# Kernel tuning notes

Measured on AMD Instinct MI355X. Metric: run time of the kernel, lower is better.

The kernel has to match this reference:

```python
import jax, jax.numpy as jnp
import numpy as np

B, S, HID = 2, 2048, 3072
NH, NKV, HD = 16, 8, 256
N_REP = NH // NKV
BITS, BLK = 4, 128
THETA = 10000.0
NEG = -1e9


def quantize_bfp(x, bits=BITS, block_size=BLK):
    """Block-floating-point quantization: blocks of `block_size` along the last
    (head_dim) axis share one power-of-two exponent; mantissas get `bits` levels
    (sign + bits-1), round-to-nearest."""
    shape = x.shape
    xb = x.reshape(-1, block_size)
    maxabs = jnp.max(jnp.abs(xb), axis=-1, keepdims=True)
    e = jnp.floor(jnp.log2(jnp.maximum(maxabs, 1e-30)))
    scale = jnp.exp2(e - (bits - 2))  # largest mantissa ~ 2^(bits-1)-1 covers maxabs
    qmax = 2.0 ** (bits - 1) - 1.0
    q = jnp.clip(jnp.round(xb / scale), -qmax, qmax) * scale
    q = jnp.where(maxabs > 0, q, 0.0)
    return q.reshape(shape)


def rotate_half(x):
    x1, x2 = jnp.split(x, 2, axis=-1)
    return jnp.concatenate((-x2, x1), axis=-1)


def setup_inputs() -> dict:
    key = jax.random.key(0)
    ks = jax.random.split(key, 5)
    hidden_states = jax.random.normal(ks[0], (B, S, HID), dtype=jnp.float32)
    sd = 0.02
    Wq = jax.random.normal(ks[1], (NH * HD, HID), dtype=jnp.float32) * sd
    Wk = jax.random.normal(ks[2], (NKV * HD, HID), dtype=jnp.float32) * sd
    Wv = jax.random.normal(ks[3], (NKV * HD, HID), dtype=jnp.float32) * sd
    Wo = jax.random.normal(ks[4], (HID, NH * HD), dtype=jnp.float32) * sd
    # rotary tables (HF convention: concat(freqs, freqs))
    pos = jnp.arange(S, dtype=jnp.float32)
    inv_freq = 1.0 / (THETA ** (jnp.arange(0, HD, 2, dtype=jnp.float32) / HD))
    freqs = jnp.einsum('s,d->sd', pos, inv_freq)
    emb = jnp.concatenate((freqs, freqs), axis=-1)  # (S, HD)
    cos = jnp.cos(emb)[None]  # (1, S, HD)
    sin = jnp.sin(emb)[None]
    # additive causal mask (B, 1, S, S)
    causal = jnp.where(jnp.tril(jnp.ones((S, S), dtype=bool)), 0.0, NEG).astype(jnp.float32)
    attention_mask = jnp.broadcast_to(causal[None, None], (B, 1, S, S))
    return {"hidden_states": hidden_states, "Wq": Wq, "Wk": Wk, "Wv": Wv,
            "Wo": Wo, "cos": cos, "sin": sin, "attention_mask": attention_mask}


def reference(hidden_states, Wq, Wk, Wv, Wo, cos, sin, attention_mask):
    b, s, _ = hidden_states.shape
    q = jnp.einsum('bsh,dh->bsd', hidden_states, Wq).reshape(b, s, NH, HD).transpose(0, 2, 1, 3)
    k = jnp.einsum('bsh,dh->bsd', hidden_states, Wk).reshape(b, s, NKV, HD).transpose(0, 2, 1, 3)
    v = jnp.einsum('bsh,dh->bsd', hidden_states, Wv).reshape(b, s, NKV, HD).transpose(0, 2, 1, 3)
    # RoPE (cos/sin unsqueezed at dim 1 -> (1,1,S,HD))
    c, sn = cos[:, None], sin[:, None]
    q = q * c + rotate_half(q) * sn
    k = k * c + rotate_half(k) * sn
    # int4 BFP quantization of keys (along rows of head_dim)
    k = quantize_bfp(k)
    # GQA: repeat kv heads
    k = jnp.repeat(k, N_REP, axis=1)
    v = jnp.repeat(v, N_REP, axis=1)
    scores = jnp.einsum('bhqd,bhkd->bhqk', q, k) / jnp.sqrt(jnp.float32(HD))
    scores = scores + attention_mask
    attn = jax.nn.softmax(scores.astype(jnp.float32), axis=-1).astype(q.dtype)
    out = jnp.einsum('bhqk,bhkd->bhqd', attn, v)
    out = out.transpose(0, 2, 1, 3).reshape(b, s, NH * HD)
    return jnp.einsum('bsd,hd->bsh', out, Wo)
```

## Files before the change

### kernel.cpp

```cpp
#include <hip/hip_runtime.h>
#include <math.h>

#define Bsz 2
#define Ssz 2048
#define HIDs 3072
#define NHs 16
#define NKVs 8
#define HDs 256

typedef _Float16 f16;
typedef _Float16 f16x8 __attribute__((ext_vector_type(8)));
typedef _Float16 f16x4 __attribute__((ext_vector_type(4)));
typedef float f32x4 __attribute__((ext_vector_type(4)));

__device__ __forceinline__ void async16(const f16* g, f16* l) {
    __builtin_amdgcn_global_load_lds(
        (const __attribute__((address_space(1))) void*)g,
        (__attribute__((address_space(3))) void*)l, 16, 0, 0);
}

__device__ __forceinline__ float row_max16(float v) {
    int t;
    t = __builtin_amdgcn_mov_dpp(__float_as_int(v), 0x121, 0xf, 0xf, false);
    v = fmaxf(v, __int_as_float(t));
    t = __builtin_amdgcn_mov_dpp(__float_as_int(v), 0x122, 0xf, 0xf, false);
    v = fmaxf(v, __int_as_float(t));
    t = __builtin_amdgcn_mov_dpp(__float_as_int(v), 0x124, 0xf, 0xf, false);
    v = fmaxf(v, __int_as_float(t));
    t = __builtin_amdgcn_mov_dpp(__float_as_int(v), 0x128, 0xf, 0xf, false);
    v = fmaxf(v, __int_as_float(t));
    return v;
}
__device__ __forceinline__ float row_sum16(float v) {
    int t;
    t = __builtin_amdgcn_mov_dpp(__float_as_int(v), 0x121, 0xf, 0xf, false);
    v = v + __int_as_float(t);
    t = __builtin_amdgcn_mov_dpp(__float_as_int(v), 0x122, 0xf, 0xf, false);
    v = v + __int_as_float(t);
    t = __builtin_amdgcn_mov_dpp(__float_as_int(v), 0x124, 0xf, 0xf, false);
    v = v + __int_as_float(t);
    t = __builtin_amdgcn_mov_dpp(__float_as_int(v), 0x128, 0xf, 0xf, false);
    v = v + __int_as_float(t);
    return v;
}

#define N4_HS  3145728
#define N4_WQ  3145728
#define N4_WK  1572864
#define N4_WV  1572864
#define N4_WO  3145728
#define N4_TOT (N4_HS + N4_WQ + N4_WK + N4_WV + N4_WO)

__global__ void cast_all_kernel(const float4* __restrict__ hs, const float4* __restrict__ wq,
                                const float4* __restrict__ wk, const float4* __restrict__ wv,
                                const float4* __restrict__ wo,
                                f16x4* __restrict__ hs_h, f16x4* __restrict__ wq_h,
                                f16x4* __restrict__ wk_h, f16x4* __restrict__ wv_h,
                                f16x4* __restrict__ wo_h) {
    int i = blockIdx.x * blockDim.x + threadIdx.x;
    const float4* src; f16x4* dst; int off;
    if (i < N4_HS)                       { src = hs; dst = hs_h; off = i; }
    else if (i < N4_HS + N4_WQ)          { src = wq; dst = wq_h; off = i - N4_HS; }
    else if (i < N4_HS + N4_WQ + N4_WK)  { src = wk; dst = wk_h; off = i - (N4_HS + N4_WQ); }
    else if (i < N4_TOT - N4_WO)         { src = wv; dst = wv_h; off = i - (N4_HS + N4_WQ + N4_WK); }
    else                                 { src = wo; dst = wo_h; off = i - (N4_TOT - N4_WO); }
    float4 v = src[off];
    f16x4 r;
    r[0] = (f16)v.x; r[1] = (f16)v.y; r[2] = (f16)v.z; r[3] = (f16)v.w;
    dst[off] = r;
}

__global__ __launch_bounds__(256) void gemm_nt_f16(
    const f16* __restrict__ A, const f16* __restrict__ Bm, float* __restrict__ C,
    int M, int N, int K)
{
    __shared__ __align__(16) f16 As[128 * 32];
    __shared__ __align__(16) f16 Bs[128 * 32];
    const int tid  = threadIdx.x;
    const int wave = tid >> 6, lane = tid & 63;
    const int l15  = lane & 15, quad = lane >> 4;
    const int m0 = blockIdx.y * 128, n0 = blockIdx.x * 128;
    const int wm = (wave >> 1) * 64, wn = (wave & 1) * 64;
    const int srow = wave * 32 + (lane >> 2);
    const int scol = (lane & 3) * 8;

    f32x4 acc[4][4];
    const f32x4 fz = {0.f, 0.f, 0.f, 0.f};
#pragma unroll
    for (int i = 0; i < 4; i++)
#pragma unroll
        for (int j = 0; j < 4; j++) acc[i][j] = fz;

    const f16* Ag0 = A  + (size_t)(m0 + srow) * K + scol;
    const f16* Ag1 = A  + (size_t)(m0 + srow + 16) * K + scol;
    const f16* Bg0 = Bm + (size_t)(n0 + srow) * K + scol;
    const f16* Bg1 = Bm + (size_t)(n0 + srow + 16) * K + scol;
    f16* Al0 = As + (wave * 32) * 32;
    f16* Al1 = As + (wave * 32 + 16) * 32;
    f16* Bl0 = Bs + (wave * 32) * 32;
    f16* Bl1 = Bs + (wave * 32 + 16) * 32;

    for (int k0 = 0; k0 < K; k0 += 32) {
        __syncthreads();
        async16(Ag0 + k0, Al0);
        async16(Ag1 + k0, Al1);
        async16(Bg0 + k0, Bl0);
        async16(Bg1 + k0, Bl1);
        __syncthreads();
        f16x8 af[4], bfr[4];
#pragma unroll
        for (int i = 0; i < 4; i++)
            af[i] = *(const f16x8*)(As + (wm + i * 16 + l15) * 32 + quad * 8);
#pragma unroll
        for (int j = 0; j < 4; j++)
            bfr[j] = *(const f16x8*)(Bs + (wn + j * 16 + l15) * 32 + quad * 8);
#pragma unroll
        for (int i = 0; i < 4; i++)
#pragma unroll
            for (int j = 0; j < 4; j++)
                acc[i][j] = __builtin_amdgcn_mfma_f32_16x16x32_f16(af[i], bfr[j], acc[i][j], 0, 0, 0);
    }
#pragma unroll
    for (int i = 0; i < 4; i++) {
        const int r = m0 + wm + i * 16 + quad * 4;
#pragma unroll
        for (int j = 0; j < 4; j++) {
            const int c = n0 + wn + j * 16 + l15;
#pragma unroll
            for (int rr = 0; rr < 4; rr++)
                C[(size_t)(r + rr) * N + c] = acc[i][j][rr];
        }
    }
}

__global__ void rope_q_kernel(const float* __restrict__ qp, const float* __restrict__ cosb,
                              const float* __restrict__ sinb, f16* __restrict__ qo) {
    const int s = blockIdx.x, h = blockIdx.y, b = blockIdx.z;
    const int d = threadIdx.x;
    const float* row = qp + (size_t)(b * Ssz + s) * (NHs * HDs) + h * HDs;
    float x = row[d];
    float other = (d < 128) ? -row[d + 128] : row[d - 128];
    float val = (x * cosb[s * HDs + d] + other * sinb[s * HDs + d]) * 0.0625f;
    qo[((size_t)(b * NHs + h) * Ssz + s) * HDs + d] = (f16)val;
}

__global__ void rope_quant_k_kernel(const float* __restrict__ kp, const float* __restrict__ cosb,
                                    const float* __restrict__ sinb, f16* __restrict__ ko) {
    const int s = blockIdx.x, h = blockIdx.y, b = blockIdx.z;
    const int d = threadIdx.x;
    const float* row = kp + (size_t)(b * Ssz + s) * (NKVs * HDs) + h * HDs;
    float x = row[d];
    float other = (d < 128) ? -row[d + 128] : row[d - 128];
    float val = x * cosb[s * HDs + d] + other * sinb[s * HDs + d];
    __shared__ float red[256];
    red[d] = fabsf(val);
    __syncthreads();
    for (int off = 64; off >= 1; off >>= 1) {
        if ((d & 127) < off) red[d] = fmaxf(red[d], red[d + off]);
        __syncthreads();
    }
    float maxabs = red[d & 128];
    float out;
    if (maxabs > 0.f) {
        int ex;
        frexpf(maxabs, &ex);
        float scale = ldexpf(1.0f, ex - 3);
        float q = rintf(val / scale);
        q = fminf(7.f, fmaxf(-7.f, q));
        out = q * scale;
    } else out = 0.f;
    ko[((size_t)(b * NKVs + h) * Ssz + s) * HDs + d] = (f16)out;
}

__global__ __launch_bounds__(256) void transpose_v_kernel(
    const float* __restrict__ proj, f16* __restrict__ vt)
{
    const int s0 = blockIdx.x * 64, c0 = blockIdx.y * 64, b = blockIdx.z;
    const int tid = threadIdx.x;
    __shared__ f16 T[64 * 72];
    {
        const int r = tid >> 2, cc = (tid & 3) * 16;
        const float* src = proj + (size_t)(b * Ssz + s0 + r) * (NKVs * HDs) + c0 + cc;
        f16 tmp[16];
#pragma unroll
        for (int q4 = 0; q4 < 4; q4++) {
            float4 v = *(const float4*)(src + q4 * 4);
            tmp[q4 * 4 + 0] = (f16)v.x; tmp[q4 * 4 + 1] = (f16)v.y;
            tmp[q4 * 4 + 2] = (f16)v.z; tmp[q4 * 4 + 3] = (f16)v.w;
        }
        *(f16x8*)(T + r * 72 + cc)     = *(f16x8*)(tmp);
        *(f16x8*)(T + r * 72 + cc + 8) = *(f16x8*)(tmp + 8);
    }
    __syncthreads();
    {
        const int d = tid >> 2, sc = (tid & 3) * 16;
        f16 tmp[16];
#pragma unroll
        for (int j = 0; j < 16; j++) tmp[j] = T[(sc + j) * 72 + d];
        const int col = c0 + d;
        const int kh = col >> 8, dd = col & 255;
        f16* dst = vt + ((size_t)(b * NKVs + kh) * HDs + dd) * Ssz + s0 + sc;
        *(f16x8*)(dst)     = *(f16x8*)(tmp);
        *(f16x8*)(dst + 8) = *(f16x8*)(tmp + 8);
    }
}

__global__ __launch_bounds__(512, 1) void attn_kernel(
    const f16* __restrict__ Q,
    const f16* __restrict__ Kq,
    const f16* __restrict__ Vt,
    f16* __restrict__ O)
{
    const int flat = blockIdx.x;
    const int xcd  = flat & 7;
    const int slot = flat >> 3;
    const int psel = slot >> 4;
    const int pair = (xcd << 1) | psel;
    const int b    = pair >> 3;
    const int kh   = pair & 7;
    const int sub  = slot & 15;
    const int h    = (kh << 1) | (sub >> 3);
    const int qtp  = sub & 7;
    const int c_short = qtp;
    const int c_long  = 15 - qtp;

    const int tid = threadIdx.x;
    const int wave = tid >> 6, lane = tid & 63;
    const int l15 = lane & 15, quad = lane >> 4;
    const int wrow = (wave < 4) ? (c_short * 128 + wave * 32)
                                : (c_long * 128 + (wave - 4) * 32);

    const f16* Qb  = Q  + ((size_t)(b * NHs  + h)  * Ssz) * HDs;
    const f16* Kg  = Kq + ((size_t)(b * NKVs + kh) * Ssz) * HDs;
    const f16* Vtg = Vt + ((size_t)(b * NKVs + kh) * HDs) * Ssz;

    __shared__ __align__(16) f16 Ks[32 * 256];
    __shared__ __align__(16) f16 Vs[256 * 32];
    __shared__ __align__(16) f16 Pl[8 * 32 * 40];
    f16* Pw = Pl + wave * 32 * 40;

    const int k_r  = lane >> 5;
    const int k_c  = lane & 31;
    const int v_r  = lane >> 2;
    const int v_gc = (lane & 3) ^ ((v_r >> 1) & 3);

    f16x8 qf0[8], qf1[8];
    {
        const f16* qrow0 = Qb + (size_t)(wrow + l15) * HDs + quad * 8;
        const f16* qrow1 = qrow0 + (size_t)16 * HDs;
#pragma unroll
        for (int ks = 0; ks < 8; ks++) {
            qf0[ks] = *(const f16x8*)(qrow0 + ks * 32);
            qf1[ks] = *(const f16x8*)(qrow1 + ks * 32);
        }
    }

    const f32x4 fz = {0.f, 0.f, 0.f, 0.f};
    f32x4 accO0[16], accO1[16];
#pragma unroll
    for (int jn = 0; jn < 16; jn++) { accO0[jn] = fz; accO1[jn] = fz; }
    float mrow0[4], mrow1[4], lp0[4], lp1[4];
#pragma unroll
    for (int r = 0; r < 4; r++) { mrow0[r] = -1e30f; mrow1[r] = -1e30f; lp0[r] = 0.f; lp1[r] = 0.f; }

    const int nk = 4 * c_long + 4;
    const int wave_max_row = wrow + 31;
    const int kswz = l15 & 7;
    const int vswz = (l15 >> 1) & 3;

    for (int kt = 0; kt < nk; kt++) {
        const int kvb = kt * 32;
        __syncthreads();
#pragma unroll
        for (int t = 0; t < 2; t++) {
            const int r2 = wave * 4 + t * 2;
            const int gc = k_c ^ ((r2 + k_r) & 7);
            async16(Kg + (size_t)(kvb + r2 + k_r) * 256 + gc * 8, Ks + r2 * 256);
        }
#pragma unroll
        for (int t = 0; t < 2; t++) {
            const int d0 = wave * 32 + t * 16;
            async16(Vtg + (size_t)(d0 + v_r) * Ssz + kvb + v_gc * 8, Vs + d0 * 32);
        }
        __syncthreads();

        if (kvb <= wave_max_row) {
            f32x4 s00 = fz, s01 = fz, s10 = fz, s11 = fz;
#pragma unroll
            for (int ks = 0; ks < 8; ks++) {
                const int cpos = ((ks * 4 + quad) ^ kswz) * 8;
                f16x8 kf0 = *(const f16x8*)(Ks + l15 * 256 + cpos);
                f16x8 kf1 = *(const f16x8*)(Ks + (16 + l15) * 256 + cpos);
                s00 = __builtin_amdgcn_mfma_f32_16x16x32_f16(qf0[ks], kf0, s00, 0, 0, 0);
                s01 = __builtin_amdgcn_mfma_f32_16x16x32_f16(qf0[ks], kf1, s01, 0, 0, 0);
                s10 = __builtin_amdgcn_mfma_f32_16x16x32_f16(qf1[ks], kf0, s10, 0, 0, 0);
                s11 = __builtin_amdgcn_mfma_f32_16x16x32_f16(qf1[ks], kf1, s11, 0, 0, 0);
            }
            float a0[4], a1[4];
            bool need = false;
            const bool diag = (kvb + 31 > wrow);
#pragma unroll
            for (int r = 0; r < 4; r++) {
                float x0 = s00[r], x1 = s01[r];
                const int row0 = wrow + quad * 4 + r;
                if (diag) {
                    if (kvb + l15 > row0)      x0 = -1e30f;
                    if (kvb + 16 + l15 > row0) x1 = -1e30f;
                }
                float rmax = row_max16(fmaxf(x0, x1));
                float mold = mrow0[r];
                bool upd = rmax > mold + 8.f;
                float mnew = upd ? rmax : mold;
                a0[r] = upd ? __expf(mold - rmax) : 1.0f;
                need = need || upd;
                float p0 = __expf(x0 - mnew);
                float p1 = __expf(x1 - mnew);
                lp0[r] = lp0[r] * a0[r] + (p0 + p1);
                mrow0[r] = mnew;
                Pw[(quad * 4 + r) * 40 + l15]      = (f16)p0;
                Pw[(quad * 4 + r) * 40 + 16 + l15] = (f16)p1;
                float y0 = s10[r], y1 = s11[r];
                const int row1 = row0 + 16;
                if (diag) {
                    if (kvb + l15 > row1)      y0 = -1e30f;
                    if (kvb + 16 + l15 > row1) y1 = -1e30f;
                }
                float rmax1 = row_max16(fmaxf(y0, y1));
                float mold1 = mrow1[r];
                bool upd1 = rmax1 > mold1 + 8.f;
                float mnew1 = upd1 ? rmax1 : mold1;
                a1[r] = upd1 ? __expf(mold1 - rmax1) : 1.0f;
                need = need || upd1;
                float q0 = __expf(y0 - mnew1);
                float q1 = __expf(y1 - mnew1);
                lp1[r] = lp1[r] * a1[r] + (q0 + q1);
                mrow1[r] = mnew1;
                Pw[(16 + quad * 4 + r) * 40 + l15]      = (f16)q0;
                Pw[(16 + quad * 4 + r) * 40 + 16 + l15] = (f16)q1;
            }
            if (__any(need)) {
#pragma unroll
                for (int jn = 0; jn < 16; jn++) {
                    f32x4 t0 = accO0[jn], t1 = accO1[jn];
                    t0[0] *= a0[0]; t0[1] *= a0[1]; t0[2] *= a0[2]; t0[3] *= a0[3];
                    t1[0] *= a1[0]; t1[1] *= a1[1]; t1[2] *= a1[2]; t1[3] *= a1[3];
                    accO0[jn] = t0; accO1[jn] = t1;
                }
            }
            f16x8 pf0 = *(const f16x8*)(Pw + l15 * 40 + quad * 8);
            f16x8 pf1 = *(const f16x8*)(Pw + (16 + l15) * 40 + quad * 8);
#pragma unroll
            for (int jn = 0; jn < 16; jn++) {
                f16x8 vf = *(const f16x8*)(Vs + (jn * 16 + l15) * 32 + (quad ^ vswz) * 8);
                accO0[jn] = __builtin_amdgcn_mfma_f32_16x16x32_f16(pf0, vf, accO0[jn], 0, 0, 0);
                accO1[jn] = __builtin_amdgcn_mfma_f32_16x16x32_f16(pf1, vf, accO1[jn], 0, 0, 0);
            }
        }
    }
#pragma unroll
    for (int r = 0; r < 4; r++) {
        const int row0 = wrow + quad * 4 + r;
        const float inv0 = 1.0f / row_sum16(lp0[r]);
        f16* orow0 = O + ((size_t)(b * Ssz) + row0) * (NHs * HDs) + h * HDs;
#pragma unroll
        for (int jn = 0; jn < 16; jn++)
            orow0[jn * 16 + l15] = (f16)(accO0[jn][r] * inv0);
        const int row1 = row0 + 16;
        const float inv1 = 1.0f / row_sum16(lp1[r]);
        f16* orow1 = O + ((size_t)(b * Ssz) + row1) * (NHs * HDs) + h * HDs;
#pragma unroll
        for (int jn = 0; jn < 16; jn++)
            orow1[jn * 16 + l15] = (f16)(accO1[jn][r] * inv1);
    }
}

extern "C" void kernel_launch(void* const* d_in, const int* in_sizes, int n_in,
                              void* d_out, int out_size, void* d_ws, size_t ws_size,
                              hipStream_t stream) {
    const float* hs   = (const float*)d_in[0];
    const float* Wq   = (const float*)d_in[1];
    const float* Wk   = (const float*)d_in[2];
    const float* Wv   = (const float*)d_in[3];
    const float* Wo   = (const float*)d_in[4];
    const float* cosb = (const float*)d_in[5];
    const float* sinb = (const float*)d_in[6];
    float* out = (float*)d_out;

    char* ws = (char*)d_ws;
    f16*   hs_h = (f16*)(ws);
    f16*   wo_h = (f16*)(ws + 25165824);
    float* proj = (float*)(ws + 50331648);
    f16*   q_h  = (f16*)(ws + 117440512);
    f16*   k_h  = (f16*)(ws + 150994944);
    f16*   vt_h = (f16*)(ws + 167772160);
    f16*   ao_h = (f16*)proj;

    cast_all_kernel<<<N4_TOT / 256, 256, 0, stream>>>(
        (const float4*)hs, (const float4*)Wq, (const float4*)Wk,
        (const float4*)Wv, (const float4*)Wo,
        (f16x4*)hs_h, (f16x4*)q_h, (f16x4*)k_h, (f16x4*)vt_h, (f16x4*)wo_h);

    gemm_nt_f16<<<dim3(4096 / 128, 4096 / 128), 256, 0, stream>>>(hs_h, q_h, proj, 4096, 4096, 3072);
    rope_q_kernel<<<dim3(Ssz, NHs, Bsz), 256, 0, stream>>>(proj, cosb, sinb, q_h);
    gemm_nt_f16<<<dim3(2048 / 128, 4096 / 128), 256, 0, stream>>>(hs_h, k_h, proj, 4096, 2048, 3072);
    rope_quant_k_kernel<<<dim3(Ssz, NKVs, Bsz), 256, 0, stream>>>(proj, cosb, sinb, k_h);
    gemm_nt_f16<<<dim3(2048 / 128, 4096 / 128), 256, 0, stream>>>(hs_h, vt_h, proj, 4096, 2048, 3072);
    transpose_v_kernel<<<dim3(Ssz / 64, (NKVs * HDs) / 64, Bsz), 256, 0, stream>>>(proj, vt_h);
    attn_kernel<<<dim3(256, 1, 1), 512, 0, stream>>>(q_h, k_h, vt_h, ao_h);
    gemm_nt_f16<<<dim3(3072 / 128, 4096 / 128), 256, 0, stream>>>(ao_h, wo_h, out, 4096, 3072, 4096);
}
```

Measured before the change: 934.3 us.

## Double-buffer K/V tiles in LDS to overlap async loads with compute

Splits the K and V shared-memory tiles into two buffers and prefetches the next 32-key tile with async global-to-LDS loads while the current tile is processed. This halves the barriers per tile and aims to hide global load latency behind the MFMA and softmax work. LDS use grows by 32 KB per block, which may lower occupancy. nk is always even (4*c_long+4), so the unrolled-by-two loop covers every tile.

```diff
diff --git a/kernel.cpp b/kernel.cpp
--- a/kernel.cpp
+++ b/kernel.cpp
@@ -234,8 +234,10 @@
     const f16* Kg  = Kq + ((size_t)(b * NKVs + kh) * Ssz) * HDs;
     const f16* Vtg = Vt + ((size_t)(b * NKVs + kh) * HDs) * Ssz;
 
-    __shared__ __align__(16) f16 Ks[32 * 256];
-    __shared__ __align__(16) f16 Vs[256 * 32];
+    __shared__ __align__(16) f16 Ks0[32 * 256];
+    __shared__ __align__(16) f16 Ks1[32 * 256];
+    __shared__ __align__(16) f16 Vs0[256 * 32];
+    __shared__ __align__(16) f16 Vs1[256 * 32];
     __shared__ __align__(16) f16 Pl[8 * 32 * 40];
     f16* Pw = Pl + wave * 32 * 40;
 
@@ -244,6 +246,21 @@
     const int v_r  = lane >> 2;
     const int v_gc = (lane & 3) ^ ((v_r >> 1) & 3);
 
+    auto stage = [&](int kt2, f16* Ksd, f16* Vsd) {
+        const int kvb_ = kt2 * 32;
+#pragma unroll
+        for (int t = 0; t < 2; t++) {
+            const int r2 = wave * 4 + t * 2;
+            const int gc = k_c ^ ((r2 + k_r) & 7);
+            async16(Kg + (size_t)(kvb_ + r2 + k_r) * 256 + gc * 8, Ksd + r2 * 256);
+        }
+#pragma unroll
+        for (int t = 0; t < 2; t++) {
+            const int d0 = wave * 32 + t * 16;
+            async16(Vtg + (size_t)(d0 + v_r) * Ssz + kvb_ + v_gc * 8, Vsd + d0 * 32);
+        }
+    };
+
     f16x8 qf0[8], qf1[8];
     {
         const f16* qrow0 = Qb + (size_t)(wrow + l15) * HDs + quad * 8;
@@ -268,95 +285,93 @@
     const int kswz = l15 & 7;
     const int vswz = (l15 >> 1) & 3;
 
-    for (int kt = 0; kt < nk; kt++) {
-        const int kvb = kt * 32;
+    auto compute = [&](int kvb, const f16* Ksc, const f16* Vsc) {
+        f32x4 s00 = fz, s01 = fz, s10 = fz, s11 = fz;
+#pragma unroll
+        for (int ks = 0; ks < 8; ks++) {
+            const int cpos = ((ks * 4 + quad) ^ kswz) * 8;
+            f16x8 kf0 = *(const f16x8*)(Ksc + l15 * 256 + cpos);
+            f16x8 kf1 = *(const f16x8*)(Ksc + (16 + l15) * 256 + cpos);
+            s00 = __builtin_amdgcn_mfma_f32_16x16x32_f16(qf0[ks], kf0, s00, 0, 0, 0);
+            s01 = __builtin_amdgcn_mfma_f32_16x16x32_f16(qf0[ks], kf1, s01, 0, 0, 0);
+            s10 = __builtin_amdgcn_mfma_f32_16x16x32_f16(qf1[ks], kf0, s10, 0, 0, 0);
+            s11 = __builtin_amdgcn_mfma_f32_16x16x32_f16(qf1[ks], kf1, s11, 0, 0, 0);
+        }
+        float a0[4], a1[4];
+        bool need = false;
+        const bool diag = (kvb + 31 > wrow);
+#pragma unroll
+        for (int r = 0; r < 4; r++) {
+            float x0 = s00[r], x1 = s01[r];
+            const int row0 = wrow + quad * 4 + r;
+            if (diag) {
+                if (kvb + l15 > row0)      x0 = -1e30f;
+                if (kvb + 16 + l15 > row0) x1 = -1e30f;
+            }
+            float rmax = row_max16(fmaxf(x0, x1));
+            float mold = mrow0[r];
+            bool upd = rmax > mold + 8.f;
+            float mnew = upd ? rmax : mold;
+            a0[r] = upd ? __expf(mold - rmax) : 1.0f;
+            need = need || upd;
+            float p0 = __expf(x0 - mnew);
+            float p1 = __expf(x1 - mnew);
+            lp0[r] = lp0[r] * a0[r] + (p0 + p1);
+            mrow0[r] = mnew;
+            Pw[(quad * 4 + r) * 40 + l15]      = (f16)p0;
+            Pw[(quad * 4 + r) * 40 + 16 + l15] = (f16)p1;
+            float y0 = s10[r], y1 = s11[r];
+            const int row1 = row0 + 16;
+            if (diag) {
+                if (kvb + l15 > row1)      y0 = -1e30f;
+                if (kvb + 16 + l15 > row1) y1 = -1e30f;
+            }
+            float rmax1 = row_max16(fmaxf(y0, y1));
+            float mold1 = mrow1[r];
+            bool upd1 = rmax1 > mold1 + 8.f;
+            float mnew1 = upd1 ? rmax1 : mold1;
+            a1[r] = upd1 ? __expf(mold1 - rmax1) : 1.0f;
+            need = need || upd1;
+            float q0 = __expf(y0 - mnew1);
+            float q1 = __expf(y1 - mnew1);
+            lp1[r] = lp1[r] * a1[r] + (q0 + q1);
+            mrow1[r] = mnew1;
+            Pw[(16 + quad * 4 + r) * 40 + l15]      = (f16)q0;
+            Pw[(16 + quad * 4 + r) * 40 + 16 + l15] = (f16)q1;
+        }
+        if (__any(need)) {
+#pragma unroll
+            for (int jn = 0; jn < 16; jn++) {
+                f32x4 t0 = accO0[jn], t1 = accO1[jn];
+                t0[0] *= a0[0]; t0[1] *= a0[1]; t0[2] *= a0[2]; t0[3] *= a0[3];
+                t1[0] *= a1[0]; t1[1] *= a1[1]; t1[2] *= a1[2]; t1[3] *= a1[3];
+                accO0[jn] = t0; accO1[jn] = t1;
+            }
+        }
+        f16x8 pf0 = *(const f16x8*)(Pw + l15 * 40 + quad * 8);
+        f16x8 pf1 = *(const f16x8*)(Pw + (16 + l15) * 40 + quad * 8);
+#pragma unroll
+        for (int jn = 0; jn < 16; jn++) {
+            f16x8 vf = *(const f16x8*)(Vsc + (jn * 16 + l15) * 32 + (quad ^ vswz) * 8);
+            accO0[jn] = __builtin_amdgcn_mfma_f32_16x16x32_f16(pf0, vf, accO0[jn], 0, 0, 0);
+            accO1[jn] = __builtin_amdgcn_mfma_f32_16x16x32_f16(pf1, vf, accO1[jn], 0, 0, 0);
+        }
+    };
+
+    stage(0, Ks0, Vs0);
+    __syncthreads();
+
+    for (int kt = 0; kt < nk; kt += 2) {
+        stage(kt + 1, Ks1, Vs1);
+        const int kvb0 = kt * 32;
+        if (kvb0 <= wave_max_row) compute(kvb0, Ks0, Vs0);
         __syncthreads();
-#pragma unroll
-        for (int t = 0; t < 2; t++) {
-            const int r2 = wave * 4 + t * 2;
-            const int gc = k_c ^ ((r2 + k_r) & 7);
-            async16(Kg + (size_t)(kvb + r2 + k_r) * 256 + gc * 8, Ks + r2 * 256);
-        }
-#pragma unroll
-        for (int t = 0; t < 2; t++) {
-            const int d0 = wave * 32 + t * 16;
-            async16(Vtg + (size_t)(d0 + v_r) * Ssz + kvb + v_gc * 8, Vs + d0 * 32);
-        }
+        if (kt + 2 < nk) stage(kt + 2, Ks0, Vs0);
+        const int kvb1 = kvb0 + 32;
+        if (kvb1 <= wave_max_row) compute(kvb1, Ks1, Vs1);
         __syncthreads();
-
-        if (kvb <= wave_max_row) {
-            f32x4 s00 = fz, s01 = fz, s10 = fz, s11 = fz;
-#pragma unroll
-            for (int ks = 0; ks < 8; ks++) {
-                const int cpos = ((ks * 4 + quad) ^ kswz) * 8;
-                f16x8 kf0 = *(const f16x8*)(Ks + l15 * 256 + cpos);
-                f16x8 kf1 = *(const f16x8*)(Ks + (16 + l15) * 256 + cpos);
-                s00 = __builtin_amdgcn_mfma_f32_16x16x32_f16(qf0[ks], kf0, s00, 0, 0, 0);
-                s01 = __builtin_amdgcn_mfma_f32_16x16x32_f16(qf0[ks], kf1, s01, 0, 0, 0);
-                s10 = __builtin_amdgcn_mfma_f32_16x16x32_f16(qf1[ks], kf0, s10, 0, 0, 0);
-                s11 = __builtin_amdgcn_mfma_f32_16x16x32_f16(qf1[ks], kf1, s11, 0, 0, 0);
-            }
-            float a0[4], a1[4];
-            bool need = false;
-            const bool diag = (kvb + 31 > wrow);
-#pragma unroll
-            for (int r = 0; r < 4; r++) {
-                float x0 = s00[r], x1 = s01[r];
-                const int row0 = wrow + quad * 4 + r;
-                if (diag) {
-                    if (kvb + l15 > row0)      x0 = -1e30f;
-                    if (kvb + 16 + l15 > row0) x1 = -1e30f;
-                }
-                float rmax = row_max16(fmaxf(x0, x1));
-                float mold = mrow0[r];
-                bool upd = rmax > mold + 8.f;
-                float mnew = upd ? rmax : mold;
-                a0[r] = upd ? __expf(mold - rmax) : 1.0f;
-                need = need || upd;
-                float p0 = __expf(x0 - mnew);
-                float p1 = __expf(x1 - mnew);
-                lp0[r] = lp0[r] * a0[r] + (p0 + p1);
-                mrow0[r] = mnew;
-                Pw[(quad * 4 + r) * 40 + l15]      = (f16)p0;
-                Pw[(quad * 4 + r) * 40 + 16 + l15] = (f16)p1;
-                float y0 = s10[r], y1 = s11[r];
-                const int row1 = row0 + 16;
-                if (diag) {
-                    if (kvb + l15 > row1)      y0 = -1e30f;
-                    if (kvb + 16 + l15 > row1) y1 = -1e30f;
-                }
-                float rmax1 = row_max16(fmaxf(y0, y1));
-                float mold1 = mrow1[r];
-                bool upd1 = rmax1 > mold1 + 8.f;
-                float mnew1 = upd1 ? rmax1 : mold1;
-                a1[r] = upd1 ? __expf(mold1 - rmax1) : 1.0f;
-                need = need || upd1;
-                float q0 = __expf(y0 - mnew1);
-                float q1 = __expf(y1 - mnew1);
-                lp1[r] = lp1[r] * a1[r] + (q0 + q1);
-                mrow1[r] = mnew1;
-                Pw[(16 + quad * 4 + r) * 40 + l15]      = (f16)q0;
-                Pw[(16 + quad * 4 + r) * 40 + 16 + l15] = (f16)q1;
-            }
-            if (__any(need)) {
-#pragma unroll
-                for (int jn = 0; jn < 16; jn++) {
-                    f32x4 t0 = accO0[jn], t1 = accO1[jn];
-                    t0[0] *= a0[0]; t0[1] *= a0[1]; t0[2] *= a0[2]; t0[3] *= a0[3];
-                    t1[0] *= a1[0]; t1[1] *= a1[1]; t1[2] *= a1[2]; t1[3] *= a1[3];
-                    accO0[jn] = t0; accO1[jn] = t1;
-                }
-            }
-            f16x8 pf0 = *(const f16x8*)(Pw + l15 * 40 + quad * 8);
-            f16x8 pf1 = *(const f16x8*)(Pw + (16 + l15) * 40 + quad * 8);
-#pragma unroll
-            for (int jn = 0; jn < 16; jn++) {
-                f16x8 vf = *(const f16x8*)(Vs + (jn * 16 + l15) * 32 + (quad ^ vswz) * 8);
-                accO0[jn] = __builtin_amdgcn_mfma_f32_16x16x32_f16(pf0, vf, accO0[jn], 0, 0, 0);
-                accO1[jn] = __builtin_amdgcn_mfma_f32_16x16x32_f16(pf1, vf, accO1[jn], 0, 0, 0);
-            }
-        }
-    }
+    }
+
 #pragma unroll
     for (int r = 0; r < 4; r++) {
         const int row0 = wrow + quad * 4 + r;
```

After: 966.6 us. 1.03x slower.

## Prefetch next K/V tile into registers during attention compute

Applied to the files above, without the earlier changes.

Replaces the direct global-to-LDS async loads of each K/V tile with a register-staged software pipeline. The next tile is loaded into registers while the current tile is computed, then written to LDS after the barrier. The aim is to hide global memory latency behind the MFMA work instead of stalling at the barrier each iteration. The cost is extra VGPRs, which may lower occupancy, plus explicit LDS store instructions.

```diff
diff --git a/kernel.cpp b/kernel.cpp
--- a/kernel.cpp
+++ b/kernel.cpp
@@ -244,6 +244,35 @@
     const int v_r  = lane >> 2;
     const int v_gc = (lane & 3) ^ ((v_r >> 1) & 3);
 
+    f16x8 krg0, krg1, vrg0, vrg1;
+    auto load_regs = [&](int kt2) {
+        const int kvb_ = kt2 * 32;
+        {
+            const int r2 = wave * 4;
+            const int gc = k_c ^ ((r2 + k_r) & 7);
+            krg0 = *(const f16x8*)(Kg + (size_t)(kvb_ + r2 + k_r) * 256 + gc * 8);
+        }
+        {
+            const int r2 = wave * 4 + 2;
+            const int gc = k_c ^ ((r2 + k_r) & 7);
+            krg1 = *(const f16x8*)(Kg + (size_t)(kvb_ + r2 + k_r) * 256 + gc * 8);
+        }
+        {
+            const int d0 = wave * 32;
+            vrg0 = *(const f16x8*)(Vtg + (size_t)(d0 + v_r) * Ssz + kvb_ + v_gc * 8);
+        }
+        {
+            const int d0 = wave * 32 + 16;
+            vrg1 = *(const f16x8*)(Vtg + (size_t)(d0 + v_r) * Ssz + kvb_ + v_gc * 8);
+        }
+    };
+    auto write_lds = [&]() {
+        *(f16x8*)(Ks + (wave * 4 + k_r) * 256 + k_c * 8)       = krg0;
+        *(f16x8*)(Ks + (wave * 4 + 2 + k_r) * 256 + k_c * 8)   = krg1;
+        *(f16x8*)(Vs + (wave * 32 + v_r) * 32 + (lane & 3) * 8)      = vrg0;
+        *(f16x8*)(Vs + (wave * 32 + 16 + v_r) * 32 + (lane & 3) * 8) = vrg1;
+    };
+
     f16x8 qf0[8], qf1[8];
     {
         const f16* qrow0 = Qb + (size_t)(wrow + l15) * HDs + quad * 8;
@@ -268,20 +297,13 @@
     const int kswz = l15 & 7;
     const int vswz = (l15 >> 1) & 3;
 
+    load_regs(0);
+
     for (int kt = 0; kt < nk; kt++) {
         const int kvb = kt * 32;
         __syncthreads();
-#pragma unroll
-        for (int t = 0; t < 2; t++) {
-            const int r2 = wave * 4 + t * 2;
-            const int gc = k_c ^ ((r2 + k_r) & 7);
-            async16(Kg + (size_t)(kvb + r2 + k_r) * 256 + gc * 8, Ks + r2 * 256);
-        }
-#pragma unroll
-        for (int t = 0; t < 2; t++) {
-            const int d0 = wave * 32 + t * 16;
-            async16(Vtg + (size_t)(d0 + v_r) * Ssz + kvb + v_gc * 8, Vs + d0 * 32);
-        }
+        write_lds();
+        if (kt + 1 < nk) load_regs(kt + 1);
         __syncthreads();
 
         if (kvb <= wave_max_row) {
```

New measurement: 946.3 us. Within noise of the previous version (+1.3%).
